# Performance work log

Hardware: AMD Instinct MI355X
Metric: run time of the kernel (lower is better)

The kernel has to match this reference:

```python
import jax, jax.numpy as jnp
import numpy as np

THRESHOLD = 0.9
EPS = 1e-12  # matches torch F.normalize eps


def setup_inputs() -> dict:
    key = jax.random.key(0)
    k1, k2 = jax.random.split(key)
    B, T, C = 16, 4096, 256
    x = jax.random.normal(k1, (B, T, C), dtype=jnp.float32)
    # 0 = valid, 1 = padded; sort so padding is trailing (realistic padded batch)
    mask = jnp.sort(jax.random.randint(k2, (B, T), 0, 2, dtype=jnp.int32), axis=1)
    return {"x": x, "mask": mask}


def reference(x, mask):
    # x: [B, T, C] float, mask: [B, T] int (0 valid, 1 padded)
    B, T, C = x.shape
    # L2-normalize along channels (F.normalize semantics: divide by max(norm, eps))
    norm = jnp.sqrt(jnp.sum(x * x, axis=-1, keepdims=True))
    x_n = x / jnp.maximum(norm, EPS)
    # cosine similarity between consecutive frames: [B, T-1]
    sim = jnp.sum(x_n[:, :-1] * x_n[:, 1:], axis=-1)
    valid_pairs = (mask[:, :-1] == 0) & (mask[:, 1:] == 0)
    is_boundary = (sim < THRESHOLD) & valid_pairs
    # segment start flags: first position starts a segment if valid
    starts = jnp.concatenate([mask[:, :1] == 0, is_boundary], axis=1)  # [B, T]
    seg_ids = jnp.cumsum(starts.astype(jnp.int32), axis=1) - 1          # [B, T]
    seg_ids = jnp.where(mask == 1, -1, seg_ids)
    # Static upper bound on segments per row is T (jit-friendly padding;
    # torch version trims to the data-dependent max, padded tail has new_mask==1)
    S = T
    offsets = jnp.arange(B, dtype=jnp.int32)[:, None] * S
    # invalid positions -> out-of-range id, dropped by segment_sum
    flat_ids = jnp.where(seg_ids >= 0, seg_ids + offsets, B * S).reshape(-1)
    sums = jax.ops.segment_sum(x.reshape(-1, C), flat_ids, num_segments=B * S)
    counts = jax.ops.segment_sum((seg_ids >= 0).astype(jnp.int32).reshape(-1),
                                 flat_ids, num_segments=B * S)
    sums = sums.reshape(B, S, C)
    counts = counts.reshape(B, S)
    pooled_x = sums / jnp.maximum(counts, 1)[..., None].astype(x.dtype)
    durations = counts.astype(jnp.int32)
    new_mask = (counts == 0).astype(jnp.int32)
    return pooled_x, durations, new_mask
```

## Files before the change

### kernel.cpp

```cpp
#include <hip/hip_runtime.h>


constexpr int B_ = 16;
constexpr int T_ = 4096;
constexpr int C_ = 256;
constexpr float THRESH = 0.9f;

__device__ __forceinline__ float dot4(const float4& a, const float4& b) {
    return a.x * b.x + a.y * b.y + a.z * b.z + a.w * b.w;
}

constexpr int K_PAIRS = 8;
constexpr int CHUNKS  = (T_ - 1 + K_PAIRS - 1) / K_PAIRS;

__global__ void k_sim(const float* __restrict__ x, const int* __restrict__ mask,
                      int* __restrict__ starts) {
    int gw   = (blockIdx.x * blockDim.x + threadIdx.x) >> 6;
    int lane = threadIdx.x & 63;
    if (gw >= B_ * CHUNKS) return;
    int b  = gw >> 9;
    int c0 = gw & (CHUNKS - 1);
    int t0 = c0 * K_PAIRS;
    int tend = min(t0 + K_PAIRS, T_ - 1);

    const float4* xb = (const float4*)(x + (size_t)b * T_ * C_);

    int mval = 0;
    if (lane <= K_PAIRS) {
        int tt = min(t0 + lane, T_ - 1);
        mval = mask[b * T_ + tt];
    }

    float4 a = xb[(size_t)t0 * 64 + lane];
    float np = dot4(a, a);

    if (lane == 0 && t0 == 0) starts[b * T_] = (mval == 0) ? 1 : 0;

    for (int t = t0; t < tend; t++) {
        float4 c = xb[(size_t)(t + 1) * 64 + lane];
        float dd = dot4(a, c);
        float nn = dot4(c, c);
#pragma unroll
        for (int off = 32; off > 0; off >>= 1) {
            dd += __shfl_xor(dd, off);
            nn += __shfl_xor(nn, off);
        }
        if (t == t0) {
#pragma unroll
            for (int off = 32; off > 0; off >>= 1) np += __shfl_xor(np, off);
        }
        int m0 = __shfl(mval, t - t0);
        int m1 = __shfl(mval, t - t0 + 1);
        float thr = THRESH * sqrtf(np * nn);
        if (lane == 0) {
            starts[b * T_ + t + 1] = (dd < thr && m0 == 0 && m1 == 0) ? 1 : 0;
        }
        a  = c;
        np = nn;
    }
}

__global__ void k_scan(const int* __restrict__ starts, const int* __restrict__ mask,
                       int* __restrict__ seg_start_g, int* __restrict__ seg_meta,
                       float* __restrict__ dur_out, float* __restrict__ nm_out) {
    const int b   = blockIdx.x;
    const int tid = threadIdx.x;
    const int PER = 16;
    const int lane = tid & 63;
    const int wid  = tid >> 6;

    __shared__ int wsum[4], wz[4];
    __shared__ int sstart[T_];

    const int4* sp = (const int4*)(starts + b * T_ + tid * PER);
    const int4* mp = (const int4*)(mask   + b * T_ + tid * PER);

    int loc[PER];
    int sum = 0, zc = 0;
#pragma unroll
    for (int i = 0; i < 4; i++) {
        int4 v = sp[i];
        sum += v.x; loc[i * 4 + 0] = sum;
        sum += v.y; loc[i * 4 + 1] = sum;
        sum += v.z; loc[i * 4 + 2] = sum;
        sum += v.w; loc[i * 4 + 3] = sum;
        int4 m = mp[i];
        zc += (m.x == 0) + (m.y == 0) + (m.z == 0) + (m.w == 0);
    }
    const int tsum = sum;

    int incl = tsum;
#pragma unroll
    for (int off = 1; off < 64; off <<= 1) {
        int v = __shfl_up(incl, off);
        if (lane >= off) incl += v;
    }
#pragma unroll
    for (int off = 32; off > 0; off >>= 1) zc += __shfl_xor(zc, off);

    if (lane == 63) wsum[wid] = incl;
    if (lane == 0)  wz[wid]   = zc;
    __syncthreads();

    int woff = 0, vlen = 0, total = 0;
#pragma unroll
    for (int w = 0; w < 4; w++) {
        if (w < wid) woff += wsum[w];
        total += wsum[w];
        vlen  += wz[w];
    }
    const int excl = woff + incl - tsum;

#pragma unroll
    for (int i = 0; i < PER; i++) {
        int flag = loc[i] - (i ? loc[i - 1] : 0);
        if (flag) sstart[excl + loc[i] - 1] = tid * PER + i;
    }
    __syncthreads();

    const int base = b * T_ + tid * PER;
#pragma unroll
    for (int i = 0; i < PER; i++) {
        int s   = tid * PER + i;
        int cnt = 0;
        if (s < total) {
            int st = sstart[s];
            int en = (s + 1 < total) ? sstart[s + 1] : vlen;
            cnt = en - st;
            seg_start_g[base + i] = st;
        }
        dur_out[base + i] = (float)cnt;
        nm_out[base + i]  = (s < total) ? 0.0f : 1.0f;
    }
    if (tid == 0) {
        seg_meta[b * 2]     = total;
        seg_meta[b * 2 + 1] = vlen;
    }
}

__global__ void k_pool(const float* __restrict__ x, const int* __restrict__ seg_start,
                       const int* __restrict__ seg_meta, float* __restrict__ pooled) {
    int gw   = (blockIdx.x * blockDim.x + threadIdx.x) >> 6;
    int lane = threadIdx.x & 63;
    if (gw >= B_ * T_) return;
    int b = gw >> 12;
    int s = gw & (T_ - 1);

    int nseg = seg_meta[b * 2];
    float4* out = (float4*)(pooled + (size_t)(b * T_ + s) * C_);

    if (s >= nseg) {
        float4 z; z.x = 0.f; z.y = 0.f; z.z = 0.f; z.w = 0.f;
        out[lane] = z;
        return;
    }
    int vlen = seg_meta[b * 2 + 1];
    int st   = seg_start[b * T_ + s];
    int en   = (s + 1 < nseg) ? seg_start[b * T_ + s + 1] : vlen;

    float4 acc; acc.x = 0.f; acc.y = 0.f; acc.z = 0.f; acc.w = 0.f;
    for (int t = st; t < en; t++) {
        float4 v = ((const float4*)(x + (size_t)(b * T_ + t) * C_))[lane];
        acc.x += v.x; acc.y += v.y; acc.z += v.z; acc.w += v.w;
    }
    float inv = 1.0f / (float)(en - st);
    acc.x *= inv; acc.y *= inv; acc.z *= inv; acc.w *= inv;
    out[lane] = acc;
}

extern "C" void kernel_launch(void* const* d_in, const int* in_sizes, int n_in,
                              void* d_out, int out_size, void* d_ws, size_t ws_size,
                              hipStream_t stream) {
    const float* x    = (const float*)d_in[0];
    const int*   mask = (const int*)d_in[1];

    float* out    = (float*)d_out;
    float* pooled = out;
    float* dur    = out + (size_t)B_ * T_ * C_;
    float* nm     = dur + (size_t)B_ * T_;

    int* starts    = (int*)d_ws;
    int* seg_start = starts + B_ * T_;
    int* seg_meta  = seg_start + B_ * T_;

    {
        int waves   = B_ * CHUNKS;
        int threads = 256;
        int blocks  = (waves * 64 + threads - 1) / threads;
        k_sim<<<blocks, threads, 0, stream>>>(x, mask, starts);
    }
    k_scan<<<B_, 256, 0, stream>>>(starts, mask, seg_start, seg_meta, dur, nm);
    {
        int waves  = B_ * T_;
        int blocks = waves * 64 / 256;
        k_pool<<<blocks, 256, 0, stream>>>(x, seg_start, seg_meta, pooled);
    }
}
```

Baseline: 128.9 us.

## Skip similarity work on padded pairs and widen scan block to 1024 threads

The similarity kernel now builds a wave ballot over the mask to count the leading valid pairs in each chunk. It writes zeros for the remaining pairs and returns early when none are valid, so padded frames are never loaded. Because padding is trailing, this skips loading roughly half of x in k_sim. The scan kernel is also reworked to use 1024 threads with 4 elements each instead of 256 with 16, which shortens the serial per-thread work at the cost of a 16-way cross-wave combine.

```diff
diff --git a/kernel.cpp b/kernel.cpp
--- a/kernel.cpp
+++ b/kernel.cpp
@@ -21,22 +21,28 @@
     int b  = gw >> 9;
     int c0 = gw & (CHUNKS - 1);
     int t0 = c0 * K_PAIRS;
-    int tend = min(t0 + K_PAIRS, T_ - 1);
+    int npairs = min(K_PAIRS, T_ - 1 - t0);
+
+    const int* mrow = mask + b * T_;
+    int mval = 0;
+    if (lane <= K_PAIRS) mval = mrow[min(t0 + lane, T_ - 1)];
+    int mnext = __shfl_down(mval, 1);
+
+    unsigned long long bm = __ballot(lane < npairs && mval == 0 && mnext == 0);
+    int nvalid = (int)__builtin_ctzll(~bm);
+    if (nvalid > npairs) nvalid = npairs;
+
+    if (lane == 0) {
+        if (t0 == 0) starts[b * T_] = (mval == 0) ? 1 : 0;
+        for (int t = t0 + nvalid; t < t0 + npairs; t++) starts[b * T_ + t + 1] = 0;
+    }
+    if (nvalid == 0) return;
 
     const float4* xb = (const float4*)(x + (size_t)b * T_ * C_);
-
-    int mval = 0;
-    if (lane <= K_PAIRS) {
-        int tt = min(t0 + lane, T_ - 1);
-        mval = mask[b * T_ + tt];
-    }
-
     float4 a = xb[(size_t)t0 * 64 + lane];
     float np = dot4(a, a);
 
-    if (lane == 0 && t0 == 0) starts[b * T_] = (mval == 0) ? 1 : 0;
-
-    for (int t = t0; t < tend; t++) {
+    for (int t = t0; t < t0 + nvalid; t++) {
         float4 c = xb[(size_t)(t + 1) * 64 + lane];
         float dd = dot4(a, c);
         float nn = dot4(c, c);
@@ -49,12 +55,8 @@
 #pragma unroll
             for (int off = 32; off > 0; off >>= 1) np += __shfl_xor(np, off);
         }
-        int m0 = __shfl(mval, t - t0);
-        int m1 = __shfl(mval, t - t0 + 1);
         float thr = THRESH * sqrtf(np * nn);
-        if (lane == 0) {
-            starts[b * T_ + t + 1] = (dd < thr && m0 == 0 && m1 == 0) ? 1 : 0;
-        }
+        if (lane == 0) starts[b * T_ + t + 1] = (dd < thr) ? 1 : 0;
         a  = c;
         np = nn;
     }
@@ -63,37 +65,31 @@
 __global__ void k_scan(const int* __restrict__ starts, const int* __restrict__ mask,
                        int* __restrict__ seg_start_g, int* __restrict__ seg_meta,
                        float* __restrict__ dur_out, float* __restrict__ nm_out) {
-    const int b   = blockIdx.x;
-    const int tid = threadIdx.x;
-    const int PER = 16;
+    const int b    = blockIdx.x;
+    const int tid  = threadIdx.x;
     const int lane = tid & 63;
     const int wid  = tid >> 6;
 
-    __shared__ int wsum[4], wz[4];
+    __shared__ int wsum[16], wz[16];
     __shared__ int sstart[T_];
 
-    const int4* sp = (const int4*)(starts + b * T_ + tid * PER);
-    const int4* mp = (const int4*)(mask   + b * T_ + tid * PER);
+    int4 v = ((const int4*)(starts + b * T_))[tid];
+    int4 m = ((const int4*)(mask   + b * T_))[tid];
 
-    int loc[PER];
-    int sum = 0, zc = 0;
-#pragma unroll
-    for (int i = 0; i < 4; i++) {
-        int4 v = sp[i];
-        sum += v.x; loc[i * 4 + 0] = sum;
-        sum += v.y; loc[i * 4 + 1] = sum;
-        sum += v.z; loc[i * 4 + 2] = sum;
-        sum += v.w; loc[i * 4 + 3] = sum;
-        int4 m = mp[i];
-        zc += (m.x == 0) + (m.y == 0) + (m.z == 0) + (m.w == 0);
-    }
+    int loc[4];
+    int sum = 0;
+    sum += v.x; loc[0] = sum;
+    sum += v.y; loc[1] = sum;
+    sum += v.z; loc[2] = sum;
+    sum += v.w; loc[3] = sum;
+    int zc = (m.x == 0) + (m.y == 0) + (m.z == 0) + (m.w == 0);
     const int tsum = sum;
 
     int incl = tsum;
 #pragma unroll
     for (int off = 1; off < 64; off <<= 1) {
-        int v = __shfl_up(incl, off);
-        if (lane >= off) incl += v;
+        int t = __shfl_up(incl, off);
+        if (lane >= off) incl += t;
     }
 #pragma unroll
     for (int off = 32; off > 0; off >>= 1) zc += __shfl_xor(zc, off);
@@ -102,26 +98,27 @@
     if (lane == 0)  wz[wid]   = zc;
     __syncthreads();
 
-    int woff = 0, vlen = 0, total = 0;
+    int woff = 0, total = 0, vlen = 0;
 #pragma unroll
-    for (int w = 0; w < 4; w++) {
-        if (w < wid) woff += wsum[w];
-        total += wsum[w];
+    for (int w = 0; w < 16; w++) {
+        int s = wsum[w];
+        if (w < wid) woff += s;
+        total += s;
         vlen  += wz[w];
     }
     const int excl = woff + incl - tsum;
 
 #pragma unroll
-    for (int i = 0; i < PER; i++) {
+    for (int i = 0; i < 4; i++) {
         int flag = loc[i] - (i ? loc[i - 1] : 0);
-        if (flag) sstart[excl + loc[i] - 1] = tid * PER + i;
+        if (flag) sstart[excl + loc[i] - 1] = tid * 4 + i;
     }
     __syncthreads();
 
-    const int base = b * T_ + tid * PER;
+    const int base = b * T_ + tid * 4;
 #pragma unroll
-    for (int i = 0; i < PER; i++) {
-        int s   = tid * PER + i;
+    for (int i = 0; i < 4; i++) {
+        int s   = tid * 4 + i;
         int cnt = 0;
         if (s < total) {
             int st = sstart[s];
@@ -189,7 +186,7 @@
         int blocks  = (waves * 64 + threads - 1) / threads;
         k_sim<<<blocks, threads, 0, stream>>>(x, mask, starts);
     }
-    k_scan<<<B_, 256, 0, stream>>>(starts, mask, seg_start, seg_meta, dur, nm);
+    k_scan<<<B_, 1024, 0, stream>>>(starts, mask, seg_start, seg_meta, dur, nm);
     {
         int waves  = B_ * T_;
         int blocks = waves * 64 / 256;
```

Measured after the change: 128.5 us. About the same (-0.3%).

## Skip similarity work on padded pairs and pack segment start/count for pooling

Applied to the files above, without the earlier changes.

The similarity kernel now finds which pairs in its chunk are valid using a wave ballot on the mask. It loads and dots x only for the leading run of valid pairs and writes zero start flags for the rest. This avoids reading x for padded frames, which make up about half of each row. The scan kernel writes a packed (start, count) int2 per segment, so the pool kernel reads one value instead of two starts plus metadata. In exchange the scan writes more scratch data, since it fills every slot.

```diff
diff --git a/kernel.cpp b/kernel.cpp
--- a/kernel.cpp
+++ b/kernel.cpp
@@ -21,22 +21,28 @@
     int b  = gw >> 9;
     int c0 = gw & (CHUNKS - 1);
     int t0 = c0 * K_PAIRS;
-    int tend = min(t0 + K_PAIRS, T_ - 1);
+    int npairs = min(K_PAIRS, T_ - 1 - t0);
+
+    const int* mrow = mask + b * T_;
+    int mval = 0;
+    if (lane <= K_PAIRS) mval = mrow[min(t0 + lane, T_ - 1)];
+    int mnext = __shfl_down(mval, 1);
+
+    unsigned long long bm = __ballot(lane < npairs && mval == 0 && mnext == 0);
+    int nvalid = (int)__builtin_ctzll(~bm);
+    if (nvalid > npairs) nvalid = npairs;
+
+    if (lane == 0) {
+        if (t0 == 0) starts[b * T_] = (mval == 0) ? 1 : 0;
+        for (int t = t0 + nvalid; t < t0 + npairs; t++) starts[b * T_ + t + 1] = 0;
+    }
+    if (nvalid == 0) return;
 
     const float4* xb = (const float4*)(x + (size_t)b * T_ * C_);
-
-    int mval = 0;
-    if (lane <= K_PAIRS) {
-        int tt = min(t0 + lane, T_ - 1);
-        mval = mask[b * T_ + tt];
-    }
-
     float4 a = xb[(size_t)t0 * 64 + lane];
     float np = dot4(a, a);
 
-    if (lane == 0 && t0 == 0) starts[b * T_] = (mval == 0) ? 1 : 0;
-
-    for (int t = t0; t < tend; t++) {
+    for (int t = t0; t < t0 + nvalid; t++) {
         float4 c = xb[(size_t)(t + 1) * 64 + lane];
         float dd = dot4(a, c);
         float nn = dot4(c, c);
@@ -49,19 +55,15 @@
 #pragma unroll
             for (int off = 32; off > 0; off >>= 1) np += __shfl_xor(np, off);
         }
-        int m0 = __shfl(mval, t - t0);
-        int m1 = __shfl(mval, t - t0 + 1);
         float thr = THRESH * sqrtf(np * nn);
-        if (lane == 0) {
-            starts[b * T_ + t + 1] = (dd < thr && m0 == 0 && m1 == 0) ? 1 : 0;
-        }
+        if (lane == 0) starts[b * T_ + t + 1] = (dd < thr) ? 1 : 0;
         a  = c;
         np = nn;
     }
 }
 
 __global__ void k_scan(const int* __restrict__ starts, const int* __restrict__ mask,
-                       int* __restrict__ seg_start_g, int* __restrict__ seg_meta,
+                       int2* __restrict__ seg_pack,
                        float* __restrict__ dur_out, float* __restrict__ nm_out) {
     const int b   = blockIdx.x;
     const int tid = threadIdx.x;
@@ -122,48 +124,41 @@
 #pragma unroll
     for (int i = 0; i < PER; i++) {
         int s   = tid * PER + i;
-        int cnt = 0;
+        int cnt = 0, st = 0;
         if (s < total) {
-            int st = sstart[s];
+            st  = sstart[s];
             int en = (s + 1 < total) ? sstart[s + 1] : vlen;
             cnt = en - st;
-            seg_start_g[base + i] = st;
         }
-        dur_out[base + i] = (float)cnt;
-        nm_out[base + i]  = (s < total) ? 0.0f : 1.0f;
-    }
-    if (tid == 0) {
-        seg_meta[b * 2]     = total;
-        seg_meta[b * 2 + 1] = vlen;
+        seg_pack[base + i] = make_int2(st, cnt);
+        dur_out[base + i]  = (float)cnt;
+        nm_out[base + i]   = (s < total) ? 0.0f : 1.0f;
     }
 }
 
-__global__ void k_pool(const float* __restrict__ x, const int* __restrict__ seg_start,
-                       const int* __restrict__ seg_meta, float* __restrict__ pooled) {
+__global__ void k_pool(const float* __restrict__ x, const int2* __restrict__ seg_pack,
+                       float* __restrict__ pooled) {
     int gw   = (blockIdx.x * blockDim.x + threadIdx.x) >> 6;
     int lane = threadIdx.x & 63;
     if (gw >= B_ * T_) return;
     int b = gw >> 12;
-    int s = gw & (T_ - 1);
 
-    int nseg = seg_meta[b * 2];
-    float4* out = (float4*)(pooled + (size_t)(b * T_ + s) * C_);
+    int2 sc = seg_pack[gw];
+    float4* out = (float4*)(pooled + (size_t)gw * C_);
 
-    if (s >= nseg) {
+    if (sc.y == 0) {
         float4 z; z.x = 0.f; z.y = 0.f; z.z = 0.f; z.w = 0.f;
         out[lane] = z;
         return;
     }
-    int vlen = seg_meta[b * 2 + 1];
-    int st   = seg_start[b * T_ + s];
-    int en   = (s + 1 < nseg) ? seg_start[b * T_ + s + 1] : vlen;
 
+    const float4* xb = (const float4*)(x + (size_t)b * T_ * C_);
     float4 acc; acc.x = 0.f; acc.y = 0.f; acc.z = 0.f; acc.w = 0.f;
-    for (int t = st; t < en; t++) {
-        float4 v = ((const float4*)(x + (size_t)(b * T_ + t) * C_))[lane];
+    for (int t = sc.x; t < sc.x + sc.y; t++) {
+        float4 v = xb[(size_t)t * 64 + lane];
         acc.x += v.x; acc.y += v.y; acc.z += v.z; acc.w += v.w;
     }
-    float inv = 1.0f / (float)(en - st);
+    float inv = 1.0f / (float)sc.y;
     acc.x *= inv; acc.y *= inv; acc.z *= inv; acc.w *= inv;
     out[lane] = acc;
 }
@@ -179,9 +174,8 @@
     float* dur    = out + (size_t)B_ * T_ * C_;
     float* nm     = dur + (size_t)B_ * T_;
 
-    int* starts    = (int*)d_ws;
-    int* seg_start = starts + B_ * T_;
-    int* seg_meta  = seg_start + B_ * T_;
+    int*  starts   = (int*)d_ws;
+    int2* seg_pack = (int2*)(starts + B_ * T_);
 
     {
         int waves   = B_ * CHUNKS;
@@ -189,10 +183,10 @@
         int blocks  = (waves * 64 + threads - 1) / threads;
         k_sim<<<blocks, threads, 0, stream>>>(x, mask, starts);
     }
-    k_scan<<<B_, 256, 0, stream>>>(starts, mask, seg_start, seg_meta, dur, nm);
+    k_scan<<<B_, 256, 0, stream>>>(starts, mask, seg_pack, dur, nm);
     {
         int waves  = B_ * T_;
         int blocks = waves * 64 / 256;
-        k_pool<<<blocks, 256, 0, stream>>>(x, seg_start, seg_meta, pooled);
+        k_pool<<<blocks, 256, 0, stream>>>(x, seg_pack, pooled);
     }
 }
```

Measured after the change: 128.9 us. Within noise of the previous version (+0.0%).
